# Kernel optimization log

Measured on AMD Instinct MI355X. Metric: run time of the kernel, lower is better.

The kernel has to match this reference:

```python
import jax, jax.numpy as jnp
import numpy as np

N = 100000
SEQ = 12
DIMS = [32, 64, 64, 32]


def _glorot(key, shape):
    fan_in, fan_out = shape[0], shape[1]
    lim = jnp.sqrt(6.0 / (fan_in + fan_out))
    return jax.random.uniform(key, shape, jnp.float32, -lim, lim)


def setup_inputs() -> dict:
    key = jax.random.key(0)
    ks = jax.random.split(key, 8)
    x = jax.random.normal(ks[0], (N, DIMS[0], 1), dtype=jnp.float32)
    spiral_indices = jax.random.randint(ks[1], (N, SEQ), 0, N)
    # SpiralConv i: Linear(SEQ * DIMS[i], DIMS[i+1])
    W0 = _glorot(ks[2], (SEQ * DIMS[0], DIMS[1]))
    b0 = jnp.zeros((DIMS[1],), jnp.float32)
    W1 = _glorot(ks[3], (SEQ * DIMS[1], DIMS[2]))
    b1 = jnp.zeros((DIMS[2],), jnp.float32)
    W2 = _glorot(ks[4], (SEQ * DIMS[2], DIMS[3]))
    b2 = jnp.zeros((DIMS[3],), jnp.float32)
    return {"x": x, "spiral_indices": spiral_indices,
            "W0": W0, "b0": b0, "W1": W1, "b1": b1, "W2": W2, "b2": b2}


def _spiral_conv(h, idx, W, b):
    # h: [N, C]; idx: [N, SEQ] -> gathered [N, SEQ, C] -> flat [N, SEQ*C]
    n = h.shape[0]
    g = jnp.take(h, idx, axis=0).reshape(n, -1)
    return g @ W + b


def reference(x, spiral_indices, W0, b0, W1, b1, W2, b2):
    h = x[..., 0]  # squeeze(-1): [N, C_in]
    h = jax.nn.elu(_spiral_conv(h, spiral_indices, W0, b0))
    h = jax.nn.elu(_spiral_conv(h, spiral_indices, W1, b1))
    h = _spiral_conv(h, spiral_indices, W2, b2)  # final_activation=False
    return h[:, :, None]
```

## Files before the change

### kernel.cpp

```cpp
#include <hip/hip_runtime.h>
#include <math.h>


typedef __bf16 bf16;
typedef bf16  bf16x4 __attribute__((ext_vector_type(4)));
typedef bf16  bf16x8 __attribute__((ext_vector_type(8)));
typedef float f32x4  __attribute__((ext_vector_type(4)));

template<int CIN, int COUT>
__device__ inline void pack_one(const float* __restrict__ W, bf16* __restrict__ BP, int e) {
    constexpr int NT = COUT / 16, CC = CIN / 32;
    const int f = e >> 9, r = e & 511, lane = r >> 3, j = r & 7;
    const int t = f % NT, cc = (f / NT) % CC, s = f / (NT * CC);
    const int col = t * 16 + (lane & 15);
    const int k   = s * CIN + cc * 32 + (lane >> 4) * 8 + j;
    BP[e] = (bf16)W[k * COUT + col];
}

__global__ __launch_bounds__(256)
void prep_all(const float* __restrict__ x, bf16* __restrict__ xb,
              const float* __restrict__ W0, const float* __restrict__ W1,
              const float* __restrict__ W2, bf16* __restrict__ B0,
              bf16* __restrict__ B1, bf16* __restrict__ B2, int n)
{
    const int gid = blockIdx.x * 256 + threadIdx.x;
    const int e = gid * 4;
    if (e < n * 32) {
        const f32x4 v = *reinterpret_cast<const f32x4*>(x + e);
        bf16x4 o = {(bf16)v[0], (bf16)v[1], (bf16)v[2], (bf16)v[3]};
        *reinterpret_cast<bf16x4*>(xb + e) = o;
    }
    if (gid < 384 * 64)                       pack_one<32, 64>(W0, B0, gid);
    else if (gid < 384 * 64 + 768 * 64)       pack_one<64, 64>(W1, B1, gid - 384 * 64);
    else if (gid < 384 * 64 + 768 * 64 + 768 * 32)
                                              pack_one<64, 32>(W2, B2, gid - 384 * 64 - 768 * 64);
}

template<int CIN, int COUT, bool ELU, bool NTS, typename TOUT>
__global__ __launch_bounds__(256, 5)
void spiral_mfma(const bf16* __restrict__ h, const int* __restrict__ idx,
                 const bf16* __restrict__ BP, const float* __restrict__ bias,
                 TOUT* __restrict__ out, int n)
{
    constexpr int CC  = CIN / 32;
    constexpr int NT  = COUT / 16;
    constexpr int PS  = CIN * COUT;
    constexpr int SC  = 6 / CC;
    constexpr int NCH = 12 / SC;
    constexpr int PL  = 6;

    __shared__ bf16 Bs[SC * PS];

    const int tid  = threadIdx.x;
    const int lane = tid & 63;
    const int wave = tid >> 6;
    const int m    = lane & 15;
    const int quad = lane >> 4;
    const int i0   = (blockIdx.x * 4 + wave) * 16;
    const bool valid = (i0 < n);

    const int ir = min(i0 + m, n - 1);
    const int4* ip = reinterpret_cast<const int4*>(idx + (size_t)ir * 12);
    const int4 q0 = ip[0], q1 = ip[1], q2 = ip[2];
    const int rg[12] = {q0.x,q0.y,q0.z,q0.w, q1.x,q1.y,q1.z,q1.w, q2.x,q2.y,q2.z,q2.w};

    f32x4 acc[NT] = {};

    #pragma unroll
    for (int c = 0; c < NCH; ++c) {
        if (c) __syncthreads();
        const bf16* src = BP + (size_t)c * SC * PS;
        #pragma unroll
        for (int r2 = tid; r2 < SC * PS / 8; r2 += 256)
            *reinterpret_cast<bf16x8*>(&Bs[r2 * 8]) =
                *reinterpret_cast<const bf16x8*>(&src[r2 * 8]);
        __syncthreads();

        bf16x8 a[PL];
        #pragma unroll
        for (int sl = 0; sl < SC; ++sl)
            #pragma unroll
            for (int cc = 0; cc < CC; ++cc)
                a[sl * CC + cc] = *reinterpret_cast<const bf16x8*>(
                    h + (size_t)rg[c * SC + sl] * CIN + cc * 32 + quad * 8);
        __builtin_amdgcn_sched_barrier(0);
        #pragma unroll
        for (int p = 0; p < PL; ++p)
            #pragma unroll
            for (int t = 0; t < NT; ++t) {
                const bf16x8 b = *reinterpret_cast<const bf16x8*>(
                    &Bs[(p * NT + t) * 512 + lane * 8]);
                acc[t] = __builtin_amdgcn_mfma_f32_16x16x32_bf16(a[p], b, acc[t], 0, 0, 0);
            }
    }

    if (!valid) return;

    #pragma unroll
    for (int t = 0; t < NT; ++t) {
        const int col = t * 16 + m;
        const float bv = bias[col];
        #pragma unroll
        for (int g = 0; g < 4; ++g) {
            const int row = i0 + quad * 4 + g;
            float v = acc[t][g] + bv;
            if (ELU) v = (v > 0.f) ? v : (__expf(v) - 1.f);
            if (NTS) __builtin_nontemporal_store((TOUT)v, out + (size_t)row * COUT + col);
            else     out[(size_t)row * COUT + col] = (TOUT)v;
        }
    }
}

extern "C" void kernel_launch(void* const* d_in, const int* in_sizes, int n_in,
                              void* d_out, int out_size, void* d_ws, size_t ws_size,
                              hipStream_t stream) {
    const float* x   = (const float*)d_in[0];
    const int*   idx = (const int*)d_in[1];
    const float* W0  = (const float*)d_in[2];
    const float* b0  = (const float*)d_in[3];
    const float* W1  = (const float*)d_in[4];
    const float* b1  = (const float*)d_in[5];
    const float* W2  = (const float*)d_in[6];
    const float* b2  = (const float*)d_in[7];
    float* out = (float*)d_out;

    const int n = in_sizes[0] / 32;

    bf16* xb = (bf16*)d_ws;
    bf16* h1 = xb + (size_t)n * 32;
    bf16* h2 = h1 + (size_t)n * 64;
    bf16* B0 = h2 + (size_t)n * 64;
    bf16* B1 = B0 + 384 * 64;
    bf16* B2 = B1 + 768 * 64;

    const int prep_threads = n * 8;
    prep_all<<<(prep_threads + 255) / 256, dim3(256), 0, stream>>>(x, xb, W0, W1, W2, B0, B1, B2, n);

    const int grid = (n + 63) / 64;
    spiral_mfma<32, 64, true,  false, bf16 ><<<grid, dim3(256), 0, stream>>>(xb, idx, B0, b0, h1,  n);
    spiral_mfma<64, 64, true,  false, bf16 ><<<grid, dim3(256), 0, stream>>>(h1, idx, B1, b1, h2,  n);
    spiral_mfma<64, 32, false, true,  float><<<grid, dim3(256), 0, stream>>>(h2, idx, B2, b2, out, n);
}
```

Before: 158.1 us.

## Fuse prep and three spiral layers into one persistent kernel with grid barriers

```diff
diff --git a/kernel.cpp b/kernel.cpp
--- a/kernel.cpp
+++ b/kernel.cpp
@@ -7,8 +7,52 @@
 typedef bf16  bf16x8 __attribute__((ext_vector_type(8)));
 typedef float f32x4  __attribute__((ext_vector_type(4)));
 
+__device__ __forceinline__ int aload(int* p) {
+    return __hip_atomic_load(p, __ATOMIC_ACQUIRE, __HIP_MEMORY_SCOPE_AGENT);
+}
+__device__ __forceinline__ void astore(int* p, int v) {
+    __hip_atomic_store(p, v, __ATOMIC_RELEASE, __HIP_MEMORY_SCOPE_AGENT);
+}
+
+__device__ __forceinline__ void gbar(int* bar, int nblk) {
+    __syncthreads();
+    if (threadIdx.x == 0) {
+        __threadfence();
+        const int grp  = blockIdx.x >> 4;
+        const int ngrp = (nblk + 15) >> 4;
+        const int gsz  = min(16, nblk - (grp << 4));
+        int* gcnt = bar + grp * 32;
+        int* ggen = bar + 64 * 32 + grp * 32;
+        int* rcnt = bar + 128 * 32;
+        int* rgen = bar + 128 * 32 + 32;
+        const int g = aload(ggen);
+        if (atomicAdd(gcnt, 1) == gsz - 1) {
+            astore(gcnt, 0);
+            const int rg = aload(rgen);
+            if (atomicAdd(rcnt, 1) == ngrp - 1) {
+                astore(rcnt, 0);
+                __hip_atomic_fetch_add(rgen, 1, __ATOMIC_RELEASE,
+                                       __HIP_MEMORY_SCOPE_AGENT);
+            } else {
+                int guard = 0;
+                while (aload(rgen) == rg && ++guard < (1 << 22))
+                    __builtin_amdgcn_s_sleep(2);
+            }
+            __hip_atomic_fetch_add(ggen, 1, __ATOMIC_RELEASE,
+                                   __HIP_MEMORY_SCOPE_AGENT);
+        } else {
+            int guard = 0;
+            while (aload(ggen) == g && ++guard < (1 << 22))
+                __builtin_amdgcn_s_sleep(2);
+        }
+        __threadfence();
+    }
+    __syncthreads();
+}
+
 template<int CIN, int COUT>
-__device__ inline void pack_one(const float* __restrict__ W, bf16* __restrict__ BP, int e) {
+__device__ __forceinline__ void pack_one(const float* __restrict__ W,
+                                         bf16* __restrict__ BP, int e) {
     constexpr int NT = COUT / 16, CC = CIN / 32;
     const int f = e >> 9, r = e & 511, lane = r >> 3, j = r & 7;
     const int t = f % NT, cc = (f / NT) % CC, s = f / (NT * CC);
@@ -17,30 +61,11 @@
     BP[e] = (bf16)W[k * COUT + col];
 }
 
-__global__ __launch_bounds__(256)
-void prep_all(const float* __restrict__ x, bf16* __restrict__ xb,
-              const float* __restrict__ W0, const float* __restrict__ W1,
-              const float* __restrict__ W2, bf16* __restrict__ B0,
-              bf16* __restrict__ B1, bf16* __restrict__ B2, int n)
-{
-    const int gid = blockIdx.x * 256 + threadIdx.x;
-    const int e = gid * 4;
-    if (e < n * 32) {
-        const f32x4 v = *reinterpret_cast<const f32x4*>(x + e);
-        bf16x4 o = {(bf16)v[0], (bf16)v[1], (bf16)v[2], (bf16)v[3]};
-        *reinterpret_cast<bf16x4*>(xb + e) = o;
-    }
-    if (gid < 384 * 64)                       pack_one<32, 64>(W0, B0, gid);
-    else if (gid < 384 * 64 + 768 * 64)       pack_one<64, 64>(W1, B1, gid - 384 * 64);
-    else if (gid < 384 * 64 + 768 * 64 + 768 * 32)
-                                              pack_one<64, 32>(W2, B2, gid - 384 * 64 - 768 * 64);
-}
-
 template<int CIN, int COUT, bool ELU, bool NTS, typename TOUT>
-__global__ __launch_bounds__(256, 5)
-void spiral_mfma(const bf16* __restrict__ h, const int* __restrict__ idx,
-                 const bf16* __restrict__ BP, const float* __restrict__ bias,
-                 TOUT* __restrict__ out, int n)
+__device__ __forceinline__ void layer_phase(
+    const bf16* __restrict__ h, const int* __restrict__ idx,
+    const bf16* __restrict__ BP, const float* __restrict__ bias,
+    TOUT* __restrict__ out, bf16* Bs, int n, int ntiles)
 {
     constexpr int CC  = CIN / 32;
     constexpr int NT  = COUT / 16;
@@ -49,66 +74,108 @@
     constexpr int NCH = 12 / SC;
     constexpr int PL  = 6;
 
-    __shared__ bf16 Bs[SC * PS];
-
     const int tid  = threadIdx.x;
     const int lane = tid & 63;
     const int wave = tid >> 6;
     const int m    = lane & 15;
     const int quad = lane >> 4;
-    const int i0   = (blockIdx.x * 4 + wave) * 16;
-    const bool valid = (i0 < n);
-
-    const int ir = min(i0 + m, n - 1);
-    const int4* ip = reinterpret_cast<const int4*>(idx + (size_t)ir * 12);
-    const int4 q0 = ip[0], q1 = ip[1], q2 = ip[2];
-    const int rg[12] = {q0.x,q0.y,q0.z,q0.w, q1.x,q1.y,q1.z,q1.w, q2.x,q2.y,q2.z,q2.w};
-
-    f32x4 acc[NT] = {};
-
-    #pragma unroll
-    for (int c = 0; c < NCH; ++c) {
-        if (c) __syncthreads();
-        const bf16* src = BP + (size_t)c * SC * PS;
+
+    for (int tile = blockIdx.x; tile < ntiles; tile += gridDim.x) {
+        const int i0 = (tile * 4 + wave) * 16;
+        const bool valid = (i0 < n);
+
+        const int ir = min(i0 + m, n - 1);
+        const int4* ip = reinterpret_cast<const int4*>(idx + (size_t)ir * 12);
+        const int4 q0 = ip[0], q1 = ip[1], q2 = ip[2];
+        const int rg[12] = {q0.x,q0.y,q0.z,q0.w, q1.x,q1.y,q1.z,q1.w,
+                            q2.x,q2.y,q2.z,q2.w};
+
+        f32x4 acc[NT] = {};
+
         #pragma unroll
-        for (int r2 = tid; r2 < SC * PS / 8; r2 += 256)
-            *reinterpret_cast<bf16x8*>(&Bs[r2 * 8]) =
-                *reinterpret_cast<const bf16x8*>(&src[r2 * 8]);
-        __syncthreads();
-
-        bf16x8 a[PL];
-        #pragma unroll
-        for (int sl = 0; sl < SC; ++sl)
-            #pragma unroll
-            for (int cc = 0; cc < CC; ++cc)
-                a[sl * CC + cc] = *reinterpret_cast<const bf16x8*>(
-                    h + (size_t)rg[c * SC + sl] * CIN + cc * 32 + quad * 8);
-        __builtin_amdgcn_sched_barrier(0);
-        #pragma unroll
-        for (int p = 0; p < PL; ++p)
+        for (int c = 0; c < NCH; ++c) {
+            __syncthreads();
+            const bf16* src = BP + (size_t)c * SC * PS;
+            #pragma unroll
+            for (int r2 = tid; r2 < SC * PS / 8; r2 += 256)
+                *reinterpret_cast<bf16x8*>(&Bs[r2 * 8]) =
+                    *reinterpret_cast<const bf16x8*>(&src[r2 * 8]);
+            __syncthreads();
+
+            bf16x8 a[PL];
+            #pragma unroll
+            for (int sl = 0; sl < SC; ++sl)
+                #pragma unroll
+                for (int cc = 0; cc < CC; ++cc)
+                    a[sl * CC + cc] = *reinterpret_cast<const bf16x8*>(
+                        h + (size_t)rg[c * SC + sl] * CIN + cc * 32 + quad * 8);
+            __builtin_amdgcn_sched_barrier(0);
+            #pragma unroll
+            for (int p = 0; p < PL; ++p)
+                #pragma unroll
+                for (int t = 0; t < NT; ++t) {
+                    const bf16x8 b = *reinterpret_cast<const bf16x8*>(
+                        &Bs[(p * NT + t) * 512 + lane * 8]);
+                    acc[t] = __builtin_amdgcn_mfma_f32_16x16x32_bf16(
+                        a[p], b, acc[t], 0, 0, 0);
+                }
+        }
+
+        if (valid) {
             #pragma unroll
             for (int t = 0; t < NT; ++t) {
-                const bf16x8 b = *reinterpret_cast<const bf16x8*>(
-                    &Bs[(p * NT + t) * 512 + lane * 8]);
-                acc[t] = __builtin_amdgcn_mfma_f32_16x16x32_bf16(a[p], b, acc[t], 0, 0, 0);
+                const int col = t * 16 + m;
+                const float bv = bias[col];
+                #pragma unroll
+                for (int g = 0; g < 4; ++g) {
+                    const int row = i0 + quad * 4 + g;
+                    float v = acc[t][g] + bv;
+                    if (ELU) v = (v > 0.f) ? v : (__expf(v) - 1.f);
+                    if (NTS) __builtin_nontemporal_store(
+                                 (TOUT)v, out + (size_t)row * COUT + col);
+                    else     out[(size_t)row * COUT + col] = (TOUT)v;
+                }
             }
-    }
-
-    if (!valid) return;
-
-    #pragma unroll
-    for (int t = 0; t < NT; ++t) {
-        const int col = t * 16 + m;
-        const float bv = bias[col];
-        #pragma unroll
-        for (int g = 0; g < 4; ++g) {
-            const int row = i0 + quad * 4 + g;
-            float v = acc[t][g] + bv;
-            if (ELU) v = (v > 0.f) ? v : (__expf(v) - 1.f);
-            if (NTS) __builtin_nontemporal_store((TOUT)v, out + (size_t)row * COUT + col);
-            else     out[(size_t)row * COUT + col] = (TOUT)v;
         }
     }
+}
+
+__global__ __launch_bounds__(256, 4)
+void fused(const float* __restrict__ x, const int* __restrict__ idx,
+           const float* __restrict__ W0, const float* __restrict__ b0,
+           const float* __restrict__ W1, const float* __restrict__ b1,
+           const float* __restrict__ W2, const float* __restrict__ b2,
+           float* __restrict__ out, bf16* __restrict__ xb,
+           bf16* __restrict__ h1, bf16* __restrict__ h2,
+           bf16* __restrict__ B0, bf16* __restrict__ B1,
+           bf16* __restrict__ B2, int* __restrict__ bar, int n)
+{
+    __shared__ bf16 Bs[12288];
+
+    const int G   = gridDim.x * 256;
+    const int gt  = blockIdx.x * 256 + threadIdx.x;
+    const int nblk = gridDim.x;
+    const int ntiles = (n + 63) / 64;
+
+    for (int u = gt; u < n * 8; u += G) {
+        const int e = u * 4;
+        const f32x4 v = *reinterpret_cast<const f32x4*>(x + e);
+        bf16x4 o = {(bf16)v[0], (bf16)v[1], (bf16)v[2], (bf16)v[3]};
+        *reinterpret_cast<bf16x4*>(xb + e) = o;
+    }
+    if (gt < 24576)                       pack_one<32, 64>(W0, B0, gt);
+    else if (gt < 24576 + 49152)          pack_one<64, 64>(W1, B1, gt - 24576);
+    else if (gt < 24576 + 49152 + 24576)  pack_one<64, 32>(W2, B2, gt - 24576 - 49152);
+
+    gbar(bar, nblk);
+
+    layer_phase<32, 64, true,  false, bf16 >(xb, idx, B0, b0, h1, Bs, n, ntiles);
+    gbar(bar, nblk);
+
+    layer_phase<64, 64, true,  false, bf16 >(h1, idx, B1, b1, h2, Bs, n, ntiles);
+    gbar(bar, nblk);
+
+    layer_phase<64, 32, false, true,  float>(h2, idx, B2, b2, out, Bs, n, ntiles);
 }
 
 extern "C" void kernel_launch(void* const* d_in, const int* in_sizes, int n_in,
@@ -133,11 +200,17 @@
     bf16* B1 = B0 + 384 * 64;
     bf16* B2 = B1 + 768 * 64;
 
-    const int prep_threads = n * 8;
-    prep_all<<<(prep_threads + 255) / 256, dim3(256), 0, stream>>>(x, xb, W0, W1, W2, B0, B1, B2, n);
-
-    const int grid = (n + 63) / 64;
-    spiral_mfma<32, 64, true,  false, bf16 ><<<grid, dim3(256), 0, stream>>>(xb, idx, B0, b0, h1,  n);
-    spiral_mfma<64, 64, true,  false, bf16 ><<<grid, dim3(256), 0, stream>>>(h1, idx, B1, b1, h2,  n);
-    spiral_mfma<64, 32, false, true,  float><<<grid, dim3(256), 0, stream>>>(h2, idx, B2, b2, out, n);
-}
+    const size_t tbl_bytes = ((size_t)n * 160 + 98304) * sizeof(bf16);
+    const size_t bar_off   = (tbl_bytes + 4095) & ~(size_t)4095;
+    int* bar = (int*)((char*)d_ws + bar_off);
+    const size_t bar_bytes = (size_t)(128 * 32 + 64) * sizeof(int);
+
+    const int ntiles = (n + 63) / 64;
+    const int grid   = (ntiles + 1) / 2;
+
+    hipMemsetAsync(bar, 0, bar_bytes, stream);
+
+    fused<<<grid, dim3(256), 0, stream>>>(
+        x, idx, W0, b0, W1, b1, W2, b2, out,
+        xb, h1, h2, B0, B1, B2, bar, n);
+}
```

Measured after the change: 600.6 us. 280% more time.
